# Performance work log

Hardware: AMD Instinct MI355X
Metric: run time of the kernel (lower is better)

## Reference

```python
import jax, jax.numpy as jnp
import numpy as np

S, D, E = 16384, 4096, 64
CAPACITY_FACTOR = 1.25  # training mode
CAPACITY = int(CAPACITY_FACTOR * S / E)  # 320


def setup_inputs() -> dict:
    key = jax.random.key(0)
    kx, kw = jax.random.split(key)
    x = jax.random.normal(kx, (S, D), dtype=jnp.float32)
    W_g = jax.random.normal(kw, (E, D), dtype=jnp.float32) * (1.0 / np.sqrt(D))
    return {"x": x, "W_g": W_g}


def reference(x, W_g):
    # Router GEMM + softmax.  x: [S, D], W_g: [E, D] (nn.Linear weight layout).
    S_ = x.shape[0]
    E_ = W_g.shape[0]
    logits = x @ W_g.T                       # [S, E]
    gates = jax.nn.softmax(logits, axis=-1)  # [S, E]

    # Top-2 experts per token (topk is constant across the original per-token loop,
    # so we compute it once).
    vals, idx = jax.lax.top_k(gates, 2)
    g1, g2 = vals[:, 0], vals[:, 1]          # [S]
    e1, e2 = idx[:, 0], idx[:, 1]            # [S] int32
    denom = g1 + g2
    g1n = g1 / denom                         # normalized top-1 gate
    g2n = g2 / denom                         # normalized top-2 gate

    # Pass 1: top-1 dispatch, capacity-limited, serialized in token order.
    # cumsum of one-hot gives each token its 1-indexed position within its expert.
    m1 = jax.nn.one_hot(e1, E_, dtype=gates.dtype)              # [S, E]
    pos1 = jnp.sum(jnp.cumsum(m1, axis=0) * m1, axis=-1)        # [S]
    keep1 = pos1 <= CAPACITY                                    # [S] bool
    counts1 = jnp.sum(m1 * keep1[:, None].astype(gates.dtype), axis=0)  # [E]

    # Pass 2: top-2 dispatch with random keep prob (rnd < 2*g2n), capacity-limited
    # against the counts remaining after pass 1, again serialized in token order.
    rnd = jax.random.uniform(jax.random.key(1), (S_,), dtype=gates.dtype)
    want2 = rnd < 2.0 * g2n                                     # [S] bool
    m2 = jax.nn.one_hot(e2, E_, dtype=gates.dtype) * want2[:, None].astype(gates.dtype)
    pos2 = jnp.sum(jnp.cumsum(m2, axis=0) * m2, axis=-1)        # [S]
    keep2 = want2 & (pos2 <= (CAPACITY - counts1)[e2])          # [S] bool

    rows = jnp.arange(S_)
    combine = jnp.zeros_like(gates)
    combine = combine.at[rows, e1].set(jnp.where(keep1, g1n, 0.0))
    combine = combine.at[rows, e2].set(jnp.where(keep2, g2n, 0.0))
    return combine
```

## Files before the change

### kernel.cpp

```cpp
#include <hip/hip_runtime.h>
#include <stdint.h>

#define S 16384
#define D 4096
#define NE 64
#define CAP 320
#define KSPLIT 4
#define KCH (D / KSPLIT)
#define TM 64
#define KB 32
#define PADLD 68
#define K2ROWS 128
#define NB (S / K2ROWS)

__device__ __forceinline__ uint32_t rotl32(uint32_t v, int n) {
  return (v << n) | (v >> (32 - n));
}

__device__ uint32_t threefry_bits(int i) {
  const uint32_t k0 = 0u, k1 = 1u;
  const uint32_t ks2 = k0 ^ k1 ^ 0x1BD11BDAu;
  uint32_t x0 = 0u + k0;
  uint32_t x1 = (uint32_t)i + k1;
#define TFR(R) { x0 += x1; x1 = rotl32(x1, R); x1 ^= x0; }
  TFR(13) TFR(15) TFR(26) TFR(6)
  x0 += k1;  x1 += ks2 + 1u;
  TFR(17) TFR(29) TFR(16) TFR(24)
  x0 += ks2; x1 += k0 + 2u;
  TFR(13) TFR(15) TFR(26) TFR(6)
  x0 += k0;  x1 += k1 + 3u;
  TFR(17) TFR(29) TFR(16) TFR(24)
  x0 += k1;  x1 += ks2 + 4u;
  TFR(13) TFR(15) TFR(26) TFR(6)
  x0 += ks2; x1 += k0 + 5u;
#undef TFR
  return x0 ^ x1;
}

__global__ __launch_bounds__(256, 4) void k1_logits(const float* __restrict__ x,
                                                    const float* __restrict__ Wg,
                                                    float* __restrict__ part) {
  __shared__ float xs[KB][PADLD];
  __shared__ float ws[KB][PADLD];
  const int kc = blockIdx.x & (KSPLIT - 1);
  const int rb = blockIdx.x >> 2;
  const int rowBase = rb * TM;
  const int kOff = kc * KCH;
  const int t = threadIdx.x;
  const int tx = t & 15;
  const int ty = t >> 4;
  const int srow = t >> 3;
  const int skq = t & 7;

  float acc[4][4];
#pragma unroll
  for (int i = 0; i < 4; ++i)
#pragma unroll
    for (int j = 0; j < 4; ++j) acc[i][j] = 0.0f;

  for (int kb = 0; kb < KCH; kb += KB) {
#pragma unroll
    for (int half = 0; half < 2; ++half) {
      const int row = srow + half * 32;
      const size_t gk = (size_t)kOff + kb + 4 * skq;
      const float4 xv = *(const float4*)&x[(size_t)(rowBase + row) * D + gk];
      const float4 wv = *(const float4*)&Wg[(size_t)row * D + gk];
      xs[4 * skq + 0][row] = xv.x;
      xs[4 * skq + 1][row] = xv.y;
      xs[4 * skq + 2][row] = xv.z;
      xs[4 * skq + 3][row] = xv.w;
      ws[4 * skq + 0][row] = wv.x;
      ws[4 * skq + 1][row] = wv.y;
      ws[4 * skq + 2][row] = wv.z;
      ws[4 * skq + 3][row] = wv.w;
    }
    __syncthreads();
#pragma unroll
    for (int kk = 0; kk < KB; ++kk) {
      const float4 xv = *(const float4*)&xs[kk][4 * ty];
      const float4 wv = *(const float4*)&ws[kk][4 * tx];
      const float xr[4] = {xv.x, xv.y, xv.z, xv.w};
      const float wr[4] = {wv.x, wv.y, wv.z, wv.w};
#pragma unroll
      for (int i = 0; i < 4; ++i)
#pragma unroll
        for (int j = 0; j < 4; ++j) acc[i][j] = fmaf(xr[i], wr[j], acc[i][j]);
    }
    __syncthreads();
  }
#pragma unroll
  for (int i = 0; i < 4; ++i) {
    float* __restrict__ po =
        part + ((size_t)kc * S + rowBase + 4 * ty + i) * NE + 4 * tx;
    *(float4*)po = make_float4(acc[i][0], acc[i][1], acc[i][2], acc[i][3]);
  }
}

__global__ __launch_bounds__(256) void k1b_reduce(const float* __restrict__ part,
                                                  int* __restrict__ E1, int* __restrict__ E2,
                                                  int* __restrict__ WANT,
                                                  float* __restrict__ G1, float* __restrict__ G2) {
  const int row = blockIdx.x * 4 + (threadIdx.x >> 6);
  const int lane = threadIdx.x & 63;
  float l = 0.0f;
#pragma unroll
  for (int c = 0; c < KSPLIT; ++c)
    l += part[((size_t)c * S + row) * NE + lane];

  float m = l;
#pragma unroll
  for (int off = 32; off; off >>= 1) m = fmaxf(m, __shfl_xor(m, off));
  float ex = expf(l - m);
  float ssum = ex;
#pragma unroll
  for (int off = 32; off; off >>= 1) ssum += __shfl_xor(ssum, off);
  ssum = __shfl(ssum, 0);
  float gate = ex / ssum;

  float v = gate; int id = lane;
#pragma unroll
  for (int off = 32; off; off >>= 1) {
    float vo = __shfl_xor(v, off); int io = __shfl_xor(id, off);
    if (vo > v || (vo == v && io < id)) { v = vo; id = io; }
  }
  const float g1 = v; const int e1 = id;
  float gate2 = (lane == e1) ? -1.0f : gate;
  v = gate2; id = lane;
#pragma unroll
  for (int off = 32; off; off >>= 1) {
    float vo = __shfl_xor(v, off); int io = __shfl_xor(id, off);
    if (vo > v || (vo == v && io < id)) { v = vo; id = io; }
  }
  const float g2 = v; const int e2 = id;

  if (lane == 0) {
    const float denom = g1 + g2;
    const float g1n = g1 / denom;
    const float g2n = g2 / denom;
    const uint32_t bits = threefry_bits(row);
    const float rnd = __uint_as_float((bits >> 9) | 0x3f800000u) - 1.0f;
    E1[row] = e1; E2[row] = e2;
    WANT[row] = (rnd < 2.0f * g2n) ? 1 : 0;
    G1[row] = g1n; G2[row] = g2n;
  }
}

__global__ __launch_bounds__(K2ROWS) void k2_rank(const int* __restrict__ E1,
                                                  const int* __restrict__ E2,
                                                  const int* __restrict__ WANT,
                                                  int* __restrict__ LR1, int* __restrict__ LR2,
                                                  int* __restrict__ H1, int* __restrict__ H2) {
  __shared__ unsigned char s1[K2ROWS], s2[K2ROWS];
  __shared__ int h1[NE], h2[NE];
  const int b = blockIdx.x, t = threadIdx.x;
  const int r = b * K2ROWS + t;
  if (t < NE) { h1[t] = 0; h2[t] = 0; }
  const int e1 = E1[r];
  const int e2 = WANT[r] ? E2[r] : NE;
  s1[t] = (unsigned char)e1;
  s2[t] = (unsigned char)e2;
  __syncthreads();
  int r1 = 0, r2 = 0;
  for (int j = 0; j < t; ++j) {
    r1 += (s1[j] == e1);
    r2 += (s2[j] == e2);
  }
  LR1[r] = r1; LR2[r] = r2;
  atomicAdd(&h1[e1], 1);
  if (e2 < NE) atomicAdd(&h2[e2], 1);
  __syncthreads();
  if (t < NE) { H1[b * NE + t] = h1[t]; H2[b * NE + t] = h2[t]; }
}

__global__ void k3_prefix(const int* __restrict__ H1, const int* __restrict__ H2,
                          int* __restrict__ OFF1, int* __restrict__ OFF2,
                          int* __restrict__ REM2) {
  const int e = threadIdx.x;
  int run1 = 0, run2 = 0;
  for (int b = 0; b < NB; ++b) {
    OFF1[b * NE + e] = run1; run1 += H1[b * NE + e];
    OFF2[b * NE + e] = run2; run2 += H2[b * NE + e];
  }
  REM2[e] = CAP - min(run1, CAP);
}

__global__ __launch_bounds__(256) void k4_scatter(const int* __restrict__ E1,
                                                  const int* __restrict__ E2,
                                                  const int* __restrict__ WANT,
                                                  const float* __restrict__ G1,
                                                  const float* __restrict__ G2,
                                                  const int* __restrict__ LR1,
                                                  const int* __restrict__ LR2,
                                                  const int* __restrict__ OFF1,
                                                  const int* __restrict__ OFF2,
                                                  const int* __restrict__ REM2,
                                                  float* __restrict__ out) {
  const int r = blockIdx.x * 256 + threadIdx.x;
  const int b = r / K2ROWS;
  const int e1 = E1[r];
  const int pos1 = OFF1[b * NE + e1] + LR1[r] + 1;
  if (pos1 <= CAP) out[(size_t)r * NE + e1] = G1[r];
  if (WANT[r]) {
    const int e2 = E2[r];
    const int pos2 = OFF2[b * NE + e2] + LR2[r] + 1;
    if (pos2 <= REM2[e2]) out[(size_t)r * NE + e2] = G2[r];
  }
}

extern "C" void kernel_launch(void* const* d_in, const int* in_sizes, int n_in,
                              void* d_out, int out_size, void* d_ws, size_t ws_size,
                              hipStream_t stream) {
  const float* x  = (const float*)d_in[0];
  const float* Wg = (const float*)d_in[1];
  float* out = (float*)d_out;
  char* ws = (char*)d_ws;

  float* part = (float*)ws;
  size_t off = (size_t)KSPLIT * S * NE * sizeof(float);
  int*   E1   = (int*)(ws + off);   off += (size_t)S * 4;
  int*   E2   = (int*)(ws + off);   off += (size_t)S * 4;
  int*   WANT = (int*)(ws + off);   off += (size_t)S * 4;
  float* G1   = (float*)(ws + off); off += (size_t)S * 4;
  float* G2   = (float*)(ws + off); off += (size_t)S * 4;
  int*   LR1  = (int*)(ws + off);   off += (size_t)S * 4;
  int*   LR2  = (int*)(ws + off);   off += (size_t)S * 4;
  int*   H1   = (int*)(ws + off);   off += (size_t)NB * NE * 4;
  int*   H2   = (int*)(ws + off);   off += (size_t)NB * NE * 4;
  int*   OFF1 = (int*)(ws + off);   off += (size_t)NB * NE * 4;
  int*   OFF2 = (int*)(ws + off);   off += (size_t)NB * NE * 4;
  int*   REM2 = (int*)(ws + off);   off += (size_t)NE * 4;

  hipMemsetAsync(d_out, 0, (size_t)out_size * sizeof(float), stream);
  k1_logits<<<(S / TM) * KSPLIT, 256, 0, stream>>>(x, Wg, part);
  k1b_reduce<<<S / 4, 256, 0, stream>>>(part, E1, E2, WANT, G1, G2);
  k2_rank<<<NB, K2ROWS, 0, stream>>>(E1, E2, WANT, LR1, LR2, H1, H2);
  k3_prefix<<<1, NE, 0, stream>>>(H1, H2, OFF1, OFF2, REM2);
  k4_scatter<<<S / 256, 256, 0, stream>>>(E1, E2, WANT, G1, G2, LR1, LR2, OFF1, OFF2, REM2, out);
}
```

Before: 427.7 us.

## Compute router GEMM with split-fp16 MFMA and fuse softmax/top-2 into it

Replaces the FP32 SIMT tiled GEMM with MFMA 32x32x16 fp16 instructions. Both operands are split into a high fp16 part and a scaled low fp16 residual, and three MFMAs per step recover near-fp32 accuracy. A small pre-kernel packs W_g into MFMA fragment layout. The k-split partial sums are now reduced in shared memory inside the same block, which also does softmax and top-2, so the partial-logit buffer and the separate reduce kernel go away. This risks small accuracy differences that could flip top-k ties and adds a per-call weight-pack launch.

```diff
diff --git a/kernel.cpp b/kernel.cpp
--- a/kernel.cpp
+++ b/kernel.cpp
@@ -5,13 +5,15 @@
 #define D 4096
 #define NE 64
 #define CAP 320
-#define KSPLIT 4
-#define KCH (D / KSPLIT)
-#define TM 64
-#define KB 32
-#define PADLD 68
+#define WQ 4
+#define KCH (D / WQ)
+#define KSTEPS (KCH / 16)
+#define NKS (D / 16)
 #define K2ROWS 128
 #define NB (S / K2ROWS)
+
+typedef _Float16 f16x8 __attribute__((ext_vector_type(8)));
+typedef float f32x16 __attribute__((ext_vector_type(16)));
 
 __device__ __forceinline__ uint32_t rotl32(uint32_t v, int n) {
   return (v << n) | (v >> (32 - n));
@@ -37,111 +39,146 @@
   return x0 ^ x1;
 }
 
-__global__ __launch_bounds__(256, 4) void k1_logits(const float* __restrict__ x,
-                                                    const float* __restrict__ Wg,
-                                                    float* __restrict__ part) {
-  __shared__ float xs[KB][PADLD];
-  __shared__ float ws[KB][PADLD];
-  const int kc = blockIdx.x & (KSPLIT - 1);
-  const int rb = blockIdx.x >> 2;
-  const int rowBase = rb * TM;
-  const int kOff = kc * KCH;
-  const int t = threadIdx.x;
-  const int tx = t & 15;
-  const int ty = t >> 4;
-  const int srow = t >> 3;
-  const int skq = t & 7;
-
-  float acc[4][4];
-#pragma unroll
-  for (int i = 0; i < 4; ++i)
-#pragma unroll
-    for (int j = 0; j < 4; ++j) acc[i][j] = 0.0f;
-
-  for (int kb = 0; kb < KCH; kb += KB) {
-#pragma unroll
-    for (int half = 0; half < 2; ++half) {
-      const int row = srow + half * 32;
-      const size_t gk = (size_t)kOff + kb + 4 * skq;
-      const float4 xv = *(const float4*)&x[(size_t)(rowBase + row) * D + gk];
-      const float4 wv = *(const float4*)&Wg[(size_t)row * D + gk];
-      xs[4 * skq + 0][row] = xv.x;
-      xs[4 * skq + 1][row] = xv.y;
-      xs[4 * skq + 2][row] = xv.z;
-      xs[4 * skq + 3][row] = xv.w;
-      ws[4 * skq + 0][row] = wv.x;
-      ws[4 * skq + 1][row] = wv.y;
-      ws[4 * skq + 2][row] = wv.z;
-      ws[4 * skq + 3][row] = wv.w;
-    }
-    __syncthreads();
-#pragma unroll
-    for (int kk = 0; kk < KB; ++kk) {
-      const float4 xv = *(const float4*)&xs[kk][4 * ty];
-      const float4 wv = *(const float4*)&ws[kk][4 * tx];
-      const float xr[4] = {xv.x, xv.y, xv.z, xv.w};
-      const float wr[4] = {wv.x, wv.y, wv.z, wv.w};
-#pragma unroll
-      for (int i = 0; i < 4; ++i)
-#pragma unroll
-        for (int j = 0; j < 4; ++j) acc[i][j] = fmaf(xr[i], wr[j], acc[i][j]);
-    }
-    __syncthreads();
-  }
-#pragma unroll
-  for (int i = 0; i < 4; ++i) {
-    float* __restrict__ po =
-        part + ((size_t)kc * S + rowBase + 4 * ty + i) * NE + 4 * tx;
-    *(float4*)po = make_float4(acc[i][0], acc[i][1], acc[i][2], acc[i][3]);
-  }
-}
-
-__global__ __launch_bounds__(256) void k1b_reduce(const float* __restrict__ part,
-                                                  int* __restrict__ E1, int* __restrict__ E2,
-                                                  int* __restrict__ WANT,
-                                                  float* __restrict__ G1, float* __restrict__ G2) {
-  const int row = blockIdx.x * 4 + (threadIdx.x >> 6);
+__global__ __launch_bounds__(256) void k0_packw(const float* __restrict__ Wg,
+                                                f16x8* __restrict__ WH,
+                                                f16x8* __restrict__ WL) {
+  const int tid = blockIdx.x * 256 + threadIdx.x;
+  const int lane = tid & 63;
+  const int t = (tid >> 6) & 1;
+  const int ks = tid >> 7;
+  const int col = 32 * t + (lane & 31);
+  const int k0 = ks * 16 + 8 * (lane >> 5);
+  const float* wp = Wg + (size_t)col * D + k0;
+  f16x8 h, l;
+#pragma unroll
+  for (int j = 0; j < 8; ++j) {
+    const float w = wp[j];
+    const _Float16 wh = (_Float16)w;
+    const float r = (w - (float)wh) * 4096.0f;
+    h[j] = wh;
+    l[j] = (_Float16)r;
+  }
+  WH[tid] = h;
+  WL[tid] = l;
+}
+
+__global__ __launch_bounds__(256) void k1_fused(const float* __restrict__ x,
+                                                const f16x8* __restrict__ WH,
+                                                const f16x8* __restrict__ WL,
+                                                int* __restrict__ E1, int* __restrict__ E2,
+                                                int* __restrict__ WANT,
+                                                float* __restrict__ G1, float* __restrict__ G2) {
+  __shared__ float lsum[WQ][32][64];
+  const int w = threadIdx.x >> 6;
   const int lane = threadIdx.x & 63;
-  float l = 0.0f;
-#pragma unroll
-  for (int c = 0; c < KSPLIT; ++c)
-    l += part[((size_t)c * S + row) * NE + lane];
-
-  float m = l;
-#pragma unroll
-  for (int off = 32; off; off >>= 1) m = fmaxf(m, __shfl_xor(m, off));
-  float ex = expf(l - m);
-  float ssum = ex;
-#pragma unroll
-  for (int off = 32; off; off >>= 1) ssum += __shfl_xor(ssum, off);
-  ssum = __shfl(ssum, 0);
-  float gate = ex / ssum;
-
-  float v = gate; int id = lane;
-#pragma unroll
-  for (int off = 32; off; off >>= 1) {
-    float vo = __shfl_xor(v, off); int io = __shfl_xor(id, off);
-    if (vo > v || (vo == v && io < id)) { v = vo; id = io; }
-  }
-  const float g1 = v; const int e1 = id;
-  float gate2 = (lane == e1) ? -1.0f : gate;
-  v = gate2; id = lane;
-#pragma unroll
-  for (int off = 32; off; off >>= 1) {
-    float vo = __shfl_xor(v, off); int io = __shfl_xor(id, off);
-    if (vo > v || (vo == v && io < id)) { v = vo; id = io; }
-  }
-  const float g2 = v; const int e2 = id;
-
-  if (lane == 0) {
-    const float denom = g1 + g2;
-    const float g1n = g1 / denom;
-    const float g2n = g2 / denom;
-    const uint32_t bits = threefry_bits(row);
-    const float rnd = __uint_as_float((bits >> 9) | 0x3f800000u) - 1.0f;
-    E1[row] = e1; E2[row] = e2;
-    WANT[row] = (rnd < 2.0f * g2n) ? 1 : 0;
-    G1[row] = g1n; G2[row] = g2n;
+  const int rowBase = blockIdx.x * 32;
+  const int row = rowBase + (lane & 31);
+  const float* xp = x + (size_t)row * D + w * KCH + (lane >> 5) * 8;
+  const int ks0 = w * KSTEPS;
+
+  f32x16 acc0[2], acc1[2];
+#pragma unroll
+  for (int t = 0; t < 2; ++t)
+#pragma unroll
+    for (int r = 0; r < 16; ++r) { acc0[t][r] = 0.0f; acc1[t][r] = 0.0f; }
+
+  float4 a0 = *(const float4*)(xp);
+  float4 a1 = *(const float4*)(xp + 4);
+#pragma unroll 2
+  for (int s = 0; s < KSTEPS; ++s) {
+    const int sn = (s + 1 < KSTEPS) ? s + 1 : s;
+    const float4 a0n = *(const float4*)(xp + sn * 16);
+    const float4 a1n = *(const float4*)(xp + sn * 16 + 4);
+    const size_t fi = (size_t)(ks0 + s) * 128 + lane;
+    const f16x8 bh0 = WH[fi];
+    const f16x8 bh1 = WH[fi + 64];
+    const f16x8 bl0 = WL[fi];
+    const f16x8 bl1 = WL[fi + 64];
+
+    const float af[8] = {a0.x, a0.y, a0.z, a0.w, a1.x, a1.y, a1.z, a1.w};
+    f16x8 ah, al;
+#pragma unroll
+    for (int j = 0; j < 8; ++j) {
+      const _Float16 h = (_Float16)af[j];
+      ah[j] = h;
+      al[j] = (_Float16)((af[j] - (float)h) * 4096.0f);
+    }
+
+    acc0[0] = __builtin_amdgcn_mfma_f32_32x32x16_f16(ah, bh0, acc0[0], 0, 0, 0);
+    acc1[0] = __builtin_amdgcn_mfma_f32_32x32x16_f16(al, bh0, acc1[0], 0, 0, 0);
+    acc1[0] = __builtin_amdgcn_mfma_f32_32x32x16_f16(ah, bl0, acc1[0], 0, 0, 0);
+    acc0[1] = __builtin_amdgcn_mfma_f32_32x32x16_f16(ah, bh1, acc0[1], 0, 0, 0);
+    acc1[1] = __builtin_amdgcn_mfma_f32_32x32x16_f16(al, bh1, acc1[1], 0, 0, 0);
+    acc1[1] = __builtin_amdgcn_mfma_f32_32x32x16_f16(ah, bl1, acc1[1], 0, 0, 0);
+
+    a0 = a0n; a1 = a1n;
+  }
+
+#pragma unroll
+  for (int t = 0; t < 2; ++t) {
+    const int col = 32 * t + (lane & 31);
+#pragma unroll
+    for (int r = 0; r < 16; ++r) {
+      const int lrow = (r & 3) + 8 * (r >> 2) + 4 * (lane >> 5);
+      lsum[w][lrow][col] = acc0[t][r] + acc1[t][r] * (1.0f / 4096.0f);
+    }
+  }
+  __syncthreads();
+
+  {
+    float* p0 = &lsum[0][0][0];
+    const float* p1 = &lsum[1][0][0];
+    const float* p2 = &lsum[2][0][0];
+    const float* p3 = &lsum[3][0][0];
+#pragma unroll
+    for (int j = 0; j < 8; ++j) {
+      const int idx = threadIdx.x + 256 * j;
+      p0[idx] = ((p0[idx] + p1[idx]) + p2[idx]) + p3[idx];
+    }
+  }
+  __syncthreads();
+
+  for (int rr = 0; rr < 8; ++rr) {
+    const int lrow = w * 8 + rr;
+    const int grow = rowBase + lrow;
+    const float l = lsum[0][lrow][lane];
+
+    float m = l;
+#pragma unroll
+    for (int off = 32; off; off >>= 1) m = fmaxf(m, __shfl_xor(m, off));
+    const float ex = expf(l - m);
+    float ssum = ex;
+#pragma unroll
+    for (int off = 32; off; off >>= 1) ssum += __shfl_xor(ssum, off);
+    ssum = __shfl(ssum, 0);
+    const float gate = ex / ssum;
+
+    float v = gate; int id = lane;
+#pragma unroll
+    for (int off = 32; off; off >>= 1) {
+      float vo = __shfl_xor(v, off); int io = __shfl_xor(id, off);
+      if (vo > v || (vo == v && io < id)) { v = vo; id = io; }
+    }
+    const float g1 = v; const int e1 = id;
+    const float gate2 = (lane == e1) ? -1.0f : gate;
+    v = gate2; id = lane;
+#pragma unroll
+    for (int off = 32; off; off >>= 1) {
+      float vo = __shfl_xor(v, off); int io = __shfl_xor(id, off);
+      if (vo > v || (vo == v && io < id)) { v = vo; id = io; }
+    }
+    const float g2 = v; const int e2 = id;
+
+    if (lane == 0) {
+      const float denom = g1 + g2;
+      const float g1n = g1 / denom;
+      const float g2n = g2 / denom;
+      const uint32_t bits = threefry_bits(grow);
+      const float rnd = __uint_as_float((bits >> 9) | 0x3f800000u) - 1.0f;
+      E1[grow] = e1; E2[grow] = e2;
+      WANT[grow] = (rnd < 2.0f * g2n) ? 1 : 0;
+      G1[grow] = g1n; G2[grow] = g2n;
+    }
   }
 }
 
@@ -215,8 +252,7 @@
   float* out = (float*)d_out;
   char* ws = (char*)d_ws;
 
-  float* part = (float*)ws;
-  size_t off = (size_t)KSPLIT * S * NE * sizeof(float);
+  size_t off = 0;
   int*   E1   = (int*)(ws + off);   off += (size_t)S * 4;
   int*   E2   = (int*)(ws + off);   off += (size_t)S * 4;
   int*   WANT = (int*)(ws + off);   off += (size_t)S * 4;
@@ -229,10 +265,12 @@
   int*   OFF1 = (int*)(ws + off);   off += (size_t)NB * NE * 4;
   int*   OFF2 = (int*)(ws + off);   off += (size_t)NB * NE * 4;
   int*   REM2 = (int*)(ws + off);   off += (size_t)NE * 4;
+  f16x8* WH   = (f16x8*)(ws + off); off += (size_t)NKS * 2 * 64 * sizeof(f16x8);
+  f16x8* WL   = (f16x8*)(ws + off); off += (size_t)NKS * 2 * 64 * sizeof(f16x8);
 
   hipMemsetAsync(d_out, 0, (size_t)out_size * sizeof(float), stream);
-  k1_logits<<<(S / TM) * KSPLIT, 256, 0, stream>>>(x, Wg, part);
-  k1b_reduce<<<S / 4, 256, 0, stream>>>(part, E1, E2, WANT, G1, G2);
+  k0_packw<<<128, 256, 0, stream>>>(Wg, WH, WL);
+  k1_fused<<<S / 32, 256, 0, stream>>>(x, WH, WL, E1, E2, WANT, G1, G2);
   k2_rank<<<NB, K2ROWS, 0, stream>>>(E1, E2, WANT, LR1, LR2, H1, H2);
   k3_prefix<<<1, NE, 0, stream>>>(H1, H2, OFF1, OFF2, REM2);
   k4_scatter<<<S / 256, 256, 0, stream>>>(E1, E2, WANT, G1, G2, LR1, LR2, OFF1, OFF2, REM2, out);
```

Result: faster. 416.6 us (-2.6%).
